# Kernel tuning notes

Hardware: AMD Instinct MI355X
Metric: run time of the kernel (lower is better)

Reference implementation:

```python
import jax, jax.numpy as jnp
import numpy as np

ATTN_SPLITS = 2
TEMPERATURE = 10000.0

# ---------- split / merge helpers (faithful to split_feature / merge_splits) ----------

def split_cf(x, ns):  # channel-first [b,c,h,w] -> [b*ns*ns, c, h/ns, w/ns]
    b, c, h, w = x.shape
    x = x.reshape(b, c, ns, h // ns, ns, w // ns).transpose(0, 2, 4, 1, 3, 5)
    return x.reshape(b * ns * ns, c, h // ns, w // ns)

def merge_cf(x, ns):  # channel-first inverse
    b, c, h, w = x.shape
    nb = b // (ns * ns)
    x = x.reshape(nb, ns, ns, c, h, w).transpose(0, 3, 1, 4, 2, 5)
    return x.reshape(nb, c, ns * h, ns * w)

def split_cl(x, ns):  # channel-last [b,h,w,c] -> [b*ns*ns, h/ns, w/ns, c]
    b, h, w, c = x.shape
    x = x.reshape(b, ns, h // ns, ns, w // ns, c).transpose(0, 1, 3, 2, 4, 5)
    return x.reshape(b * ns * ns, h // ns, w // ns, c)

def merge_cl(x, ns):  # channel-last inverse
    b, h, w, c = x.shape
    nb = b // (ns * ns)
    x = x.reshape(nb, ns, ns, h, w, c).transpose(0, 1, 3, 2, 4, 5)
    return x.reshape(nb, ns * h, ns * w, c)

# ---------- PositionEmbeddingSine (normalize=True, scale=2*pi) ----------

def pos_embed_sine(h, w, num_pos_feats):
    scale = 2.0 * np.pi
    eps = 1e-6
    ones = jnp.ones((h, w), jnp.float32)
    y_embed = jnp.cumsum(ones, 0)
    x_embed = jnp.cumsum(ones, 1)
    y_embed = y_embed / (y_embed[-1:, :] + eps) * scale
    x_embed = x_embed / (x_embed[:, -1:] + eps) * scale
    dim_t = jnp.arange(num_pos_feats, dtype=jnp.float32)
    dim_t = TEMPERATURE ** (2.0 * jnp.floor(dim_t / 2.0) / num_pos_feats)
    pos_x = x_embed[:, :, None] / dim_t  # [h,w,npf]
    pos_y = y_embed[:, :, None] / dim_t
    pos_x = jnp.stack([jnp.sin(pos_x[:, :, 0::2]), jnp.cos(pos_x[:, :, 1::2])], -1).reshape(h, w, -1)
    pos_y = jnp.stack([jnp.sin(pos_y[:, :, 0::2]), jnp.cos(pos_y[:, :, 1::2])], -1).reshape(h, w, -1)
    pos = jnp.concatenate([pos_y, pos_x], -1)  # [h,w,c]
    return jnp.transpose(pos, (2, 0, 1))[None]  # [1,c,h,w]

def feature_add_position(f0, f1, attn_splits, c):
    if attn_splits > 1:
        f0s = split_cf(f0, attn_splits)
        f1s = split_cf(f1, attn_splits)
        pos = pos_embed_sine(f0s.shape[2], f0s.shape[3], c // 2)
        return merge_cf(f0s + pos, attn_splits), merge_cf(f1s + pos, attn_splits)
    pos = pos_embed_sine(f0.shape[2], f0.shape[3], c // 2)
    return f0 + pos, f1 + pos

# ---------- shifted-window attention mask (static, numpy) ----------

def shift_window_attn_mask(h, w, ns):
    wsh, wsw = h // ns, w // ns
    ssh, ssw = wsh // 2, wsw // 2
    img = np.zeros((h, w), np.float32)
    cnt = 0
    for hs in (slice(0, -wsh), slice(-wsh, -ssh), slice(-ssh, None)):
        for ws in (slice(0, -wsw), slice(-wsw, -ssw), slice(-ssw, None)):
            img[hs, ws] = cnt
            cnt += 1
    m = img.reshape(ns, wsh, ns, wsw).transpose(0, 2, 1, 3).reshape(ns * ns, wsh * wsw)
    am = m[:, None, :] - m[:, :, None]
    am = np.where(am != 0, -100.0, 0.0).astype(np.float32)
    return jnp.asarray(am)  # [ns*ns, N, N]

# ---------- single-head split (shifted) window attention ----------

def split_window_attention(q, k, v, ns, h, w, attn_mask):
    b, _, c = q.shape
    bn = b * ns * ns
    wsh, wsw = h // ns, w // ns
    ssh, ssw = wsh // 2, wsw // 2
    q = q.reshape(b, h, w, c)
    k = k.reshape(b, h, w, c)
    v = v.reshape(b, h, w, c)
    q = jnp.roll(q, (-ssh, -ssw), (1, 2))
    k = jnp.roll(k, (-ssh, -ssw), (1, 2))
    v = jnp.roll(v, (-ssh, -ssw), (1, 2))
    qs = split_cl(q, ns).reshape(bn, -1, c)
    ks = split_cl(k, ns).reshape(bn, -1, c)
    vs = split_cl(v, ns).reshape(bn, -1, c)
    scores = jnp.einsum('bnc,bmc->bnm', qs, ks) / jnp.sqrt(jnp.asarray(c, qs.dtype))
    scores = scores + jnp.tile(attn_mask, (b, 1, 1))
    attn = jax.nn.softmax(scores, axis=-1)
    out = jnp.einsum('bnm,bmc->bnc', attn, vs)
    out = merge_cl(out.reshape(bn, wsh, wsw, c), ns)
    out = jnp.roll(out, (ssh, ssw), (1, 2))
    return out.reshape(b, -1, c)

# ---------- global correlation softmax matching ----------

def global_correlation_softmax(f0, f1):
    b, c, h, w = f0.shape
    f0v = f0.reshape(b, c, -1)  # [b,c,hw]
    f1v = f1.reshape(b, c, -1)
    corr = jnp.einsum('bcn,bcm->bnm', f0v, f1v) / jnp.sqrt(jnp.asarray(c, f0.dtype))
    yy, xx = jnp.meshgrid(jnp.arange(h), jnp.arange(w), indexing='ij')
    grid = jnp.stack([xx, yy], 0).astype(f0.dtype)  # [2,h,w] (x,y)
    gridv = grid.reshape(2, -1).T  # [hw,2]
    prob = jax.nn.softmax(corr, axis=-1)
    corresp = jnp.einsum('bnm,md->bnd', prob, gridv).reshape(b, h, w, 2).transpose(0, 3, 1, 2)
    flow = corresp - grid[None]
    return flow

# ---------- setup & reference ----------

def setup_inputs() -> dict:
    key = jax.random.key(0)
    k0, k1 = jax.random.split(key)
    b, c, h, w = 4, 128, 64, 64
    feature0 = jax.random.normal(k0, (b, c, h, w), jnp.float32)
    feature1 = jax.random.normal(k1, (b, c, h, w), jnp.float32)
    return {'feature0': feature0, 'feature1': feature1}

def reference(feature0, feature1):
    b, c, h, w = feature0.shape
    ns = ATTN_SPLITS
    f0, f1 = feature_add_position(feature0, feature1, ns, c)
    attn_mask = shift_window_attn_mask(h, w, ns)
    q = f0.reshape(b, c, -1).transpose(0, 2, 1)  # [b,hw,c]
    kv = f1.reshape(b, c, -1).transpose(0, 2, 1)
    f0_attn = split_window_attention(q, kv, kv, ns, h, w, attn_mask)  # [b,hw,c]
    f0_attn = f0_attn.transpose(0, 2, 1).reshape(b, c, h, w)
    flow = global_correlation_softmax(f0_attn, f1)  # [b,2,h,w]
    return flow
```

## Files before the change

kernel.cpp:

```cpp
#include <hip/hip_runtime.h>
#include <hip/hip_bf16.h>
#include <math.h>

#define NB 4
#define NC 128
#define NH 64
#define NW 64
#define NHW 4096
#define SCALE 0.08838834764831845f
#define PSL2E 0.12753102543365835f

typedef short bf16x8 __attribute__((ext_vector_type(8)));
typedef float f32x4 __attribute__((ext_vector_type(4)));

__device__ __forceinline__ unsigned bfbits(float f) {
    unsigned u = __float_as_uint(f);
    return (u + 0x7FFFu + ((u >> 16) & 1u)) >> 16;
}
__device__ __forceinline__ unsigned bfpair(float a, float b) {
    return bfbits(a) | (bfbits(b) << 16);
}

__global__ __launch_bounds__(256) void pos_kernel(float* __restrict__ pos) {
    int idx = blockIdx.x * 256 + threadIdx.x;
    if (idx >= NC * 32 * 32) return;
    int x = idx & 31;
    int y = (idx >> 5) & 31;
    int c = idx >> 10;
    const float twopi = 6.283185307179586f;
    const float denom = 32.0f + 1e-6f;
    int cc = (c < 64) ? c : (c - 64);
    float e = (c < 64) ? (float)(y + 1) : (float)(x + 1);
    e = e * (twopi / denom);
    int k = cc >> 1;
    float arg = e * exp2f(-0.41524101186091903f * (float)k);
    pos[idx] = (cc & 1) ? cosf(arg) : sinf(arg);
}

__global__ __launch_bounds__(256) void pack_kernel(
        const float* __restrict__ f0, const float* __restrict__ f1,
        const float* __restrict__ pos,
        __hip_bfloat16* __restrict__ F0t, __hip_bfloat16* __restrict__ Bt,
        __hip_bfloat16* __restrict__ Ktw) {
    __shared__ float T[64][129];
    int blk = blockIdx.x;
    const bool isA = blk < 256;
    const float* src = isA ? f0 : f1;
    blk &= 255;
    const int y = blk & 63;
    const int b = blk >> 6;
    const int tid = threadIdx.x;
    const float* s = src + (size_t)b * NC * NHW + y * 64;
    const float sA = isA ? PSL2E : 1.0f;
    for (int idx = tid; idx < 64 * NC; idx += 256) {
        const int x = idx & 63, c = idx >> 6;
        T[x][c] = (s[c * NHW + x] + pos[(c << 10) + ((y & 31) << 5) + (x & 31)]) * sA;
    }
    __syncthreads();
    __hip_bfloat16* dst = isA ? F0t : Bt;
    for (int idx = tid; idx < 512; idx += 256) {
        const int x = idx >> 3, c0 = (idx & 7) * 16;
        const float* tr = &T[x][c0];
        uint4 v0, v1;
        v0.x = bfpair(tr[0], tr[1]);   v0.y = bfpair(tr[2], tr[3]);
        v0.z = bfpair(tr[4], tr[5]);   v0.w = bfpair(tr[6], tr[7]);
        v1.x = bfpair(tr[8], tr[9]);   v1.y = bfpair(tr[10], tr[11]);
        v1.z = bfpair(tr[12], tr[13]); v1.w = bfpair(tr[14], tr[15]);
        __hip_bfloat16* row = dst + ((size_t)b * NHW + y * 64 + x) * NC + c0;
        *reinterpret_cast<uint4*>(row) = v0;
        *reinterpret_cast<uint4*>(row + 8) = v1;
    }
    if (!isA) {
        const int yp = (y + 48) & 63;
        const int wi = yp >> 5, ry = yp & 31;
        const int c = tid >> 1;
        const int wj = tid & 1;
        const int win = b * 4 + wi * 2 + wj;
        unsigned up[16];
        #pragma unroll
        for (int pr = 0; pr < 16; ++pr) {
            const int x0 = ((wj << 5) + 2 * pr + 16) & 63;
            up[pr] = bfpair(T[x0][c], T[x0 + 1][c]);
        }
        __hip_bfloat16* krow = Ktw + ((size_t)win * NC + c) * 1024 + ry * 32;
        uint4* uv = reinterpret_cast<uint4*>(up);
        #pragma unroll
        for (int i = 0; i < 4; ++i)
            *reinterpret_cast<uint4*>(krow + i * 8) = uv[i];
    }
}

__global__ __launch_bounds__(256) void attn_mfma_kernel(
        const __hip_bfloat16* __restrict__ F0t,
        const __hip_bfloat16* __restrict__ Bt,
        const __hip_bfloat16* __restrict__ Ktw,
        __hip_bfloat16* __restrict__ At) {
    __shared__ __align__(16) char lds[73728];
    char* Pscr = lds + 65536;
    const int tid = threadIdx.x;
    const int lane = tid & 63;
    const int w = tid >> 6;
    const int p = w & 1;
    const int qh = w >> 1;
    const int l15 = lane & 15;
    const int g = lane >> 4;
    const int blk = blockIdx.x;
    const int win = blk >> 5;
    const int qt32 = blk & 31;
    const int b = win >> 2, wi = (win >> 1) & 1, wj = win & 1;

    const char* Btb = (const char*)(Bt + (size_t)b * NHW * NC);
    const char* Vsrc = (const char*)(Ktw + (size_t)win * NC * 1024);

    bf16x8 qf[4];
    {
        const int tok = qt32 * 32 + qh * 16 + l15;
        const int yo = ((wi << 5) + (tok >> 5) + 16) & 63;
        const int xo = ((wj << 5) + (tok & 31) + 16) & 63;
        const __hip_bfloat16* qrow =
            F0t + ((size_t)b * NHW + yo * 64 + xo) * NC + g * 8;
        #pragma unroll
        for (int kk = 0; kk < 4; ++kk)
            qf[kk] = *reinterpret_cast<const bf16x8*>(qrow + kk * 32);
    }

    const int reg_q = (wi ? (qt32 < 16 ? 1 : 2) : 0) * 3
                    + (wj ? (qh == 0 ? 1 : 2) : 0);

    auto stageK = [&](int slot, int ktg) {
        char* dst = lds + slot * 16384;
        #pragma unroll
        for (int it = 0; it < 4; ++it) {
            const int obase = w * 4096 + it * 1024;
            const int row = w * 16 + it * 4 + (lane >> 4);
            const int tok = ktg * 64 + row;
            const int yo = ((wi << 5) + (tok >> 5) + 16) & 63;
            const int xo = ((wj << 5) + (tok & 31) + 16) & 63;
            const char* src = Btb + (yo * 64 + xo) * 256 +
                              (((lane & 15) * 16) ^ ((row & 7) << 4));
            __builtin_amdgcn_global_load_lds(
                (const __attribute__((address_space(1))) void*)src,
                (__attribute__((address_space(3))) void*)(dst + obase), 16, 0, 0);
        }
    };
    auto stageV = [&](int slot, int ktg) {
        char* dst = lds + 32768 + slot * 16384;
        #pragma unroll
        for (int it = 0; it < 4; ++it) {
            const int obase = w * 4096 + it * 1024;
            const int o = obase + lane * 16;
            const int crow = o >> 7;
            const int off = o & 127;
            __builtin_amdgcn_global_load_lds(
                (const __attribute__((address_space(1))) void*)(Vsrc + crow * 2048 + ktg * 128 + (off ^ ((crow & 7) << 4))),
                (__attribute__((address_space(3))) void*)(dst + obase), 16, 0, 0);
        }
    };

    f32x4 oacc[8] = {{0,0,0,0},{0,0,0,0},{0,0,0,0},{0,0,0,0},
                     {0,0,0,0},{0,0,0,0},{0,0,0,0},{0,0,0,0}};
    float zacc = 0.f;

    for (int s = 0; s < 8; ++s) {
        __syncthreads();
        stageK(0, 2 * s); stageK(1, 2 * s + 1);
        stageV(0, 2 * s); stageV(1, 2 * s + 1);
        __syncthreads();

        const int ktg = 2 * s + p;
        const char* kb = lds + p * 16384;
        f32x4 sacc[4] = {{0,0,0,0},{0,0,0,0},{0,0,0,0},{0,0,0,0}};
        #pragma unroll
        for (int kk = 0; kk < 4; ++kk) {
            #pragma unroll
            for (int msub = 0; msub < 4; ++msub) {
                const int byte = msub * 4096 + l15 * 256 + ((kk * 64 + g * 16) ^ ((l15 & 7) << 4));
                bf16x8 kf = *reinterpret_cast<const bf16x8*>(kb + byte);
                sacc[msub] = __builtin_amdgcn_mfma_f32_16x16x32_bf16(kf, qf[kk], sacc[msub], 0, 0, 0);
            }
        }

        const int rk_row = (wi ? (ktg < 8 ? 1 : 2) : 0) * 3;
        char* pw = Pscr + w * 2048;
        #pragma unroll
        for (int msub = 0; msub < 4; ++msub) {
            const int rk = rk_row + (wj ? ((msub & 1) == 0 ? 1 : 2) : 0);
            const bool ok = (rk == reg_q);
            const float p0 = ok ? exp2f(sacc[msub][0]) : 0.f;
            const float p1 = ok ? exp2f(sacc[msub][1]) : 0.f;
            const float p2 = ok ? exp2f(sacc[msub][2]) : 0.f;
            const float p3 = ok ? exp2f(sacc[msub][3]) : 0.f;
            zacc += (p0 + p1) + (p2 + p3);
            *reinterpret_cast<unsigned*>(pw + l15 * 128 + ((msub * 32 + g * 8 + 0) ^ ((l15 & 7) << 4))) = bfpair(p0, p1);
            *reinterpret_cast<unsigned*>(pw + l15 * 128 + ((msub * 32 + g * 8 + 4) ^ ((l15 & 7) << 4))) = bfpair(p2, p3);
        }
        bf16x8 pf[2];
        #pragma unroll
        for (int kk = 0; kk < 2; ++kk)
            pf[kk] = *reinterpret_cast<const bf16x8*>(pw + l15 * 128 + ((kk * 64 + g * 16) ^ ((l15 & 7) << 4)));

        const char* vb = lds + 32768 + p * 16384;
        #pragma unroll
        for (int kk = 0; kk < 2; ++kk) {
            #pragma unroll
            for (int co = 0; co < 8; ++co) {
                const int byte = (co * 16 + l15) * 128 + ((kk * 64 + g * 16) ^ ((l15 & 7) << 4));
                bf16x8 vf = *reinterpret_cast<const bf16x8*>(vb + byte);
                oacc[co] = __builtin_amdgcn_mfma_f32_16x16x32_bf16(pf[kk], vf, oacc[co], 0, 0, 0);
            }
        }
    }
    __syncthreads();

    float z = zacc;
    z += __shfl_xor(z, 16);
    z += __shfl_xor(z, 32);

    float* zl = (float*)(lds + 16384);
    if (p == 1) {
        float* od = (float*)(lds + qh * 8192);
        #pragma unroll
        for (int r = 0; r < 4; ++r) {
            #pragma unroll
            for (int co = 0; co < 8; ++co)
                od[(g * 4 + r) * 128 + co * 16 + l15] = oacc[co][r];
        }
        if (lane < 16) zl[qh * 16 + lane] = z;
    }
    __syncthreads();
    if (p == 0) {
        const float* od = (const float*)(lds + qh * 8192);
        const float zc = z + zl[qh * 16 + l15];
        unsigned short* olds = (unsigned short*)(lds + 16896 + qh * 4096);
        #pragma unroll
        for (int r = 0; r < 4; ++r) {
            const float zi = PSL2E / __shfl(zc, g * 4 + r);
            #pragma unroll
            for (int co = 0; co < 8; ++co) {
                const float o = oacc[co][r] + od[(g * 4 + r) * 128 + co * 16 + l15];
                olds[(g * 4 + r) * 128 + co * 16 + l15] = (unsigned short)bfbits(o * zi);
            }
        }
        const int qloc = lane >> 2;
        const int c0 = (lane & 3) * 32;
        const int tok = qt32 * 32 + qh * 16 + qloc;
        const int yo = ((wi << 5) + (tok >> 5) + 16) & 63;
        const int xo = ((wj << 5) + (tok & 31) + 16) & 63;
        __hip_bfloat16* arow = At + ((size_t)b * NHW + yo * 64 + xo) * NC + c0;
        #pragma unroll
        for (int i = 0; i < 4; ++i) {
            int4 v = *reinterpret_cast<const int4*>(olds + qloc * 128 + c0 + i * 8);
            *reinterpret_cast<int4*>(arow + i * 8) = v;
        }
    }
}

__global__ __launch_bounds__(256) void corr_part_kernel(
        const __hip_bfloat16* __restrict__ At,
        const __hip_bfloat16* __restrict__ Bt,
        float4* __restrict__ part) {
    __shared__ __hip_bfloat16 Bs[2][64 * 128];
    const int tid = threadIdx.x;
    const int lane = tid & 63;
    const int w = tid >> 6;
    const int blk = blockIdx.x;
    const int ms = blk & 7;
    const int nt = (blk >> 3) & 31;
    const int b = blk >> 8;
    const int l15 = lane & 15;
    const int g = lane >> 4;
    const int n0 = nt * 128 + w * 32;

    const __hip_bfloat16* Ab = At + (size_t)b * NHW * NC;
    const __hip_bfloat16* Bb = Bt + (size_t)b * NHW * NC;

    bf16x8 afrag[2][4];
    #pragma unroll
    for (int s = 0; s < 2; ++s) {
        const __hip_bfloat16* arow = Ab + (size_t)(n0 + s * 16 + l15) * NC + g * 8;
        #pragma unroll
        for (int kk = 0; kk < 4; ++kk)
            afrag[s][kk] = *reinterpret_cast<const bf16x8*>(arow + kk * 32);
    }

    auto stage = [&](int buf, int mtile) {
        const char* srcbase = reinterpret_cast<const char*>(Bb + (size_t)mtile * 64 * NC);
        #pragma unroll
        for (int it = 0; it < 4; ++it) {
            const int obase = w * 4096 + it * 1024;
            const int o = obase + lane * 16;
            const int row = o >> 8;
            const int off = o & 255;
            const char* src = srcbase + row * 256 + (off ^ ((row & 7) << 4));
            __builtin_amdgcn_global_load_lds(
                (const __attribute__((address_space(1))) void*)src,
                (__attribute__((address_space(3))) void*)((char*)&Bs[buf][0] + obase),
                16, 0, 0);
        }
    };

    f32x4 rl[2]  = {{0,0,0,0},{0,0,0,0}};
    f32x4 rsm[2] = {{0,0,0,0},{0,0,0,0}};
    f32x4 rsy[2] = {{0,0,0,0},{0,0,0,0}};

    stage(0, ms * 8);
    __syncthreads();

    for (int mt = 0; mt < 8; ++mt) {
        const int buf = mt & 1;
        if (mt < 7) stage(buf ^ 1, ms * 8 + mt + 1);

        f32x4 acc[2][4] = {{{0,0,0,0},{0,0,0,0},{0,0,0,0},{0,0,0,0}},
                           {{0,0,0,0},{0,0,0,0},{0,0,0,0},{0,0,0,0}}};
        const char* base = (const char*)&Bs[buf][0];
        #pragma unroll
        for (int kk = 0; kk < 4; ++kk) {
            #pragma unroll
            for (int msub = 0; msub < 4; ++msub) {
                const int byte = msub * 4096 + l15 * 256 +
                                 ((kk * 64 + g * 16) ^ ((l15 & 7) << 4));
                bf16x8 bfrag = *reinterpret_cast<const bf16x8*>(base + byte);
                acc[0][msub] = __builtin_amdgcn_mfma_f32_16x16x32_bf16(
                    afrag[0][kk], bfrag, acc[0][msub], 0, 0, 0);
                acc[1][msub] = __builtin_amdgcn_mfma_f32_16x16x32_bf16(
                    afrag[1][kk], bfrag, acc[1][msub], 0, 0, 0);
            }
        }
        const float y0 = (float)(ms * 8 + mt);
        #pragma unroll
        for (int s = 0; s < 2; ++s) {
            #pragma unroll
            for (int r = 0; r < 4; ++r) {
                float p0 = exp2f(acc[s][0][r]);
                float p1 = exp2f(acc[s][1][r]);
                float p2 = exp2f(acc[s][2][r]);
                float p3 = exp2f(acc[s][3][r]);
                float ts = (p0 + p1) + (p2 + p3);
                rl[s][r]  += ts;
                rsy[s][r] += y0 * ts;
                rsm[s][r] += fmaf(3.f, p3, fmaf(2.f, p2, p1));
            }
        }
        __syncthreads();
    }

    const float xl = (float)l15;
    #pragma unroll
    for (int s = 0; s < 2; ++s) {
        #pragma unroll
        for (int r = 0; r < 4; ++r) {
            float a  = rl[s][r];
            float sx = xl * rl[s][r] + 16.f * rsm[s][r];
            float sy = rsy[s][r];
            #pragma unroll
            for (int m = 1; m < 16; m <<= 1) {
                a  += __shfl_xor(a, m);
                sx += __shfl_xor(sx, m);
                sy += __shfl_xor(sy, m);
            }
            if (l15 == 0) {
                const int n = n0 + s * 16 + g * 4 + r;
                part[((size_t)b * NHW + n) * 8 + ms] = make_float4(a, sx, sy, 0.f);
            }
        }
    }
}

__global__ __launch_bounds__(256) void finalize_kernel(
        const float4* __restrict__ part, float* __restrict__ out) {
    const int idx = blockIdx.x * 256 + threadIdx.x;
    if (idx >= NB * NHW) return;
    const int n = idx & (NHW - 1);
    const int b = idx >> 12;
    float l = 0.f, sx = 0.f, sy = 0.f;
    #pragma unroll
    for (int i = 0; i < 8; ++i) {
        float4 p = part[(size_t)idx * 8 + i];
        l += p.x; sx += p.y; sy += p.z;
    }
    const float inv = 1.0f / l;
    out[(size_t)b * 2 * NHW + n]       = sx * inv - (float)(n & 63);
    out[(size_t)b * 2 * NHW + NHW + n] = sy * inv - (float)(n >> 6);
}

extern "C" void kernel_launch(void* const* d_in, const int* in_sizes, int n_in,
                              void* d_out, int out_size, void* d_ws, size_t ws_size,
                              hipStream_t stream) {
    const float* f0 = (const float*)d_in[0];
    const float* f1 = (const float*)d_in[1];
    float* pos = (float*)d_ws;
    __hip_bfloat16* F0t = (__hip_bfloat16*)(pos + 131072);
    __hip_bfloat16* Bt  = F0t + (size_t)NB * NHW * NC;
    __hip_bfloat16* Ktw = Bt  + (size_t)NB * NHW * NC;
    __hip_bfloat16* At  = Ktw + (size_t)16 * NC * 1024;
    float4* part = (float4*)(At + (size_t)NB * NHW * NC);
    float* out = (float*)d_out;

    pos_kernel<<<512, 256, 0, stream>>>(pos);
    pack_kernel<<<512, 256, 0, stream>>>(f0, f1, pos, F0t, Bt, Ktw);
    attn_mfma_kernel<<<512, 256, 0, stream>>>(F0t, Bt, Ktw, At);
    corr_part_kernel<<<1024, 256, 0, stream>>>(At, Bt, part);
    finalize_kernel<<<64, 256, 0, stream>>>(part, out);
}
```

Measured before the change: 79.22 us.

## Drop LDS staging in correlation kernel, load B fragments directly from global

The correlation kernel no longer double-buffers key tiles through shared memory with async global-to-LDS loads and barriers. Each wave now reads its B fragments straight from global memory, relying on L1/L2 for reuse. Each wave also covers 64 query rows instead of 32, which halves the grid and doubles the A fragments and accumulators held in registers. This removes LDS traffic and block-wide synchronisation. In exchange it adds redundant global/L2 reads across waves, raises register pressure, and loses the explicit prefetch overlap.

```diff
diff --git a/kernel.cpp b/kernel.cpp
--- a/kernel.cpp
+++ b/kernel.cpp
@@ -259,94 +259,72 @@
         const __hip_bfloat16* __restrict__ At,
         const __hip_bfloat16* __restrict__ Bt,
         float4* __restrict__ part) {
-    __shared__ __hip_bfloat16 Bs[2][64 * 128];
     const int tid = threadIdx.x;
     const int lane = tid & 63;
     const int w = tid >> 6;
     const int blk = blockIdx.x;
     const int ms = blk & 7;
-    const int nt = (blk >> 3) & 31;
-    const int b = blk >> 8;
+    const int nt = (blk >> 3) & 15;
+    const int b = blk >> 7;
     const int l15 = lane & 15;
     const int g = lane >> 4;
-    const int n0 = nt * 128 + w * 32;
+    const int n0 = nt * 256 + w * 64;
 
     const __hip_bfloat16* Ab = At + (size_t)b * NHW * NC;
-    const __hip_bfloat16* Bb = Bt + (size_t)b * NHW * NC;
-
-    bf16x8 afrag[2][4];
+    const char* Bb = (const char*)(Bt + (size_t)b * NHW * NC);
+
+    bf16x8 afrag[4][4];
     #pragma unroll
-    for (int s = 0; s < 2; ++s) {
+    for (int s = 0; s < 4; ++s) {
         const __hip_bfloat16* arow = Ab + (size_t)(n0 + s * 16 + l15) * NC + g * 8;
         #pragma unroll
         for (int kk = 0; kk < 4; ++kk)
             afrag[s][kk] = *reinterpret_cast<const bf16x8*>(arow + kk * 32);
     }
 
-    auto stage = [&](int buf, int mtile) {
-        const char* srcbase = reinterpret_cast<const char*>(Bb + (size_t)mtile * 64 * NC);
-        #pragma unroll
-        for (int it = 0; it < 4; ++it) {
-            const int obase = w * 4096 + it * 1024;
-            const int o = obase + lane * 16;
-            const int row = o >> 8;
-            const int off = o & 255;
-            const char* src = srcbase + row * 256 + (off ^ ((row & 7) << 4));
-            __builtin_amdgcn_global_load_lds(
-                (const __attribute__((address_space(1))) void*)src,
-                (__attribute__((address_space(3))) void*)((char*)&Bs[buf][0] + obase),
-                16, 0, 0);
-        }
-    };
-
-    f32x4 rl[2]  = {{0,0,0,0},{0,0,0,0}};
-    f32x4 rsm[2] = {{0,0,0,0},{0,0,0,0}};
-    f32x4 rsy[2] = {{0,0,0,0},{0,0,0,0}};
-
-    stage(0, ms * 8);
-    __syncthreads();
+    f32x4 rl[4]  = {{0,0,0,0},{0,0,0,0},{0,0,0,0},{0,0,0,0}};
+    f32x4 rsm[4] = {{0,0,0,0},{0,0,0,0},{0,0,0,0},{0,0,0,0}};
+    f32x4 rsy[4] = {{0,0,0,0},{0,0,0,0},{0,0,0,0},{0,0,0,0}};
+
+    const char* bl = Bb + (size_t)ms * 512 * 256 + l15 * 256 + g * 16;
 
     for (int mt = 0; mt < 8; ++mt) {
-        const int buf = mt & 1;
-        if (mt < 7) stage(buf ^ 1, ms * 8 + mt + 1);
-
-        f32x4 acc[2][4] = {{{0,0,0,0},{0,0,0,0},{0,0,0,0},{0,0,0,0}},
-                           {{0,0,0,0},{0,0,0,0},{0,0,0,0},{0,0,0,0}}};
-        const char* base = (const char*)&Bs[buf][0];
-        #pragma unroll
-        for (int kk = 0; kk < 4; ++kk) {
-            #pragma unroll
-            for (int msub = 0; msub < 4; ++msub) {
-                const int byte = msub * 4096 + l15 * 256 +
-                                 ((kk * 64 + g * 16) ^ ((l15 & 7) << 4));
-                bf16x8 bfrag = *reinterpret_cast<const bf16x8*>(base + byte);
-                acc[0][msub] = __builtin_amdgcn_mfma_f32_16x16x32_bf16(
-                    afrag[0][kk], bfrag, acc[0][msub], 0, 0, 0);
-                acc[1][msub] = __builtin_amdgcn_mfma_f32_16x16x32_bf16(
-                    afrag[1][kk], bfrag, acc[1][msub], 0, 0, 0);
-            }
-        }
+        const char* bt = bl + (size_t)mt * 64 * 256;
+        bf16x8 bf[4][4];
+        #pragma unroll
+        for (int msub = 0; msub < 4; ++msub)
+            #pragma unroll
+            for (int kk = 0; kk < 4; ++kk)
+                bf[kk][msub] = *reinterpret_cast<const bf16x8*>(bt + msub * 4096 + kk * 64);
+
         const float y0 = (float)(ms * 8 + mt);
         #pragma unroll
-        for (int s = 0; s < 2; ++s) {
+        for (int s = 0; s < 4; ++s) {
+            f32x4 acc[4] = {{0,0,0,0},{0,0,0,0},{0,0,0,0},{0,0,0,0}};
+            #pragma unroll
+            for (int kk = 0; kk < 4; ++kk) {
+                #pragma unroll
+                for (int msub = 0; msub < 4; ++msub)
+                    acc[msub] = __builtin_amdgcn_mfma_f32_16x16x32_bf16(
+                        afrag[s][kk], bf[kk][msub], acc[msub], 0, 0, 0);
+            }
             #pragma unroll
             for (int r = 0; r < 4; ++r) {
-                float p0 = exp2f(acc[s][0][r]);
-                float p1 = exp2f(acc[s][1][r]);
-                float p2 = exp2f(acc[s][2][r]);
-                float p3 = exp2f(acc[s][3][r]);
+                float p0 = exp2f(acc[0][r]);
+                float p1 = exp2f(acc[1][r]);
+                float p2 = exp2f(acc[2][r]);
+                float p3 = exp2f(acc[3][r]);
                 float ts = (p0 + p1) + (p2 + p3);
                 rl[s][r]  += ts;
                 rsy[s][r] += y0 * ts;
                 rsm[s][r] += fmaf(3.f, p3, fmaf(2.f, p2, p1));
             }
         }
-        __syncthreads();
     }
 
     const float xl = (float)l15;
     #pragma unroll
-    for (int s = 0; s < 2; ++s) {
+    for (int s = 0; s < 4; ++s) {
         #pragma unroll
         for (int r = 0; r < 4; ++r) {
             float a  = rl[s][r];
@@ -399,6 +377,6 @@
     pos_kernel<<<512, 256, 0, stream>>>(pos);
     pack_kernel<<<512, 256, 0, stream>>>(f0, f1, pos, F0t, Bt, Ktw);
     attn_mfma_kernel<<<512, 256, 0, stream>>>(F0t, Bt, Ktw, At);
-    corr_part_kernel<<<1024, 256, 0, stream>>>(At, Bt, part);
+    corr_part_kernel<<<512, 256, 0, stream>>>(At, Bt, part);
     finalize_kernel<<<64, 256, 0, stream>>>(part, out);
 }
```

Measured after the change: 111.4 us. 1.41x slower.
